# Performance work log

Hardware: AMD Instinct MI355X
Metric: run time of the kernel (lower is better)

Reference implementation:

```python
import jax, jax.numpy as jnp
import numpy as np

P = 64          # num_populations
T = 8192        # buffer_size (buffer assumed full / all valid)
K = 8           # num_bins
HIST = 2        # history_length
NPAST = K ** HIST          # number of single-series past states
NCOMB = NPAST * NPAST      # joint (y_past, x_past) states
N = T - HIST - 1           # n_samples per pair


def _discretize(x):
    # Faithful to torch _discretize: min-max normalize, floor into K bins.
    xmin = x.min()
    xmax = x.max()
    rng = xmax - xmin
    norm = (x - xmin) / (rng + 1e-8)
    b = jnp.clip((norm * (K - 1)).astype(jnp.int32), 0, K - 1)
    return jnp.where(rng < 1e-8, jnp.zeros_like(b), b)


def _cond_entropy(counts, state_mask):
    # counts: (S, K) histogram of y_future per conditioning state.
    # Torch skips states with total count < 2; weight = count/N.
    tot = counts.sum(axis=1)                          # (S,)
    valid = (tot >= 2.0) & state_mask
    p = counts / jnp.maximum(tot[:, None], 1.0)
    p_safe = jnp.where(counts > 0, p, 1.0)
    h = -jnp.where(counts > 0, p * jnp.log2(p_safe), 0.0).sum(axis=1)
    w = tot / N
    return jnp.where(valid, w * h, 0.0).sum()


def _te(src_d, tgt_d):
    # src_d, tgt_d: (T,) int bins. TE(src -> tgt) in bits.
    yf = tgt_d[HIST + 1: HIST + 1 + N]                # y_future, (N,)
    # hash of k-step histories: sum_i K**i * series[k-i : k-i+N]
    yp = sum((K ** i) * tgt_d[HIST - i: HIST - i + N] for i in range(HIST))
    xp = sum((K ** i) * src_d[HIST - i: HIST - i + N] for i in range(HIST))
    # joint histograms via scatter-add (the fused histogram kernel target)
    cy = jnp.zeros((NPAST, K), jnp.float32).at[yp, yf].add(1.0)
    cc = jnp.zeros((NCOMB, K), jnp.float32).at[yp * NPAST + xp, yf].add(1.0)
    # torch loops yp in range(min(NPAST, N)) -> mask out higher state ids
    mask_y = jnp.arange(NPAST) < min(NPAST, N)
    h_y_given_yp = _cond_entropy(cy, mask_y)
    h_y_given_ypxp = _cond_entropy(cc, jnp.ones((NCOMB,), dtype=bool))
    return jnp.maximum(0.0, h_y_given_yp - h_y_given_ypxp)


def setup_inputs() -> dict:
    key = jax.random.key(0)
    return {"time_series": jax.random.normal(key, (T, P), dtype=jnp.float32)}


def reference(time_series):
    # time_series: (T, P). Returns flow_matrix (P, P): flow[i, j] = TE(i -> j).
    d = jax.vmap(_discretize, in_axes=1, out_axes=0)(time_series)  # (P, T) int
    flow = jax.vmap(lambda s: jax.vmap(lambda t: _te(s, t))(d))(d)  # (P, P)
    return flow * (1.0 - jnp.eye(P, dtype=flow.dtype))  # diagonal forced to 0
```

## Files before the change

### kernel.cpp

```cpp
#include <hip/hip_runtime.h>

static constexpr int T = 8192;
static constexpr int P = 64;
static constexpr int NSAMP = 8189;

__global__ __launch_bounds__(1024) void prep_kernel(const float* __restrict__ ts,
        unsigned short* __restrict__ A, unsigned short* __restrict__ X,
        float* __restrict__ h_y)
{
    __shared__ float col[T];
    __shared__ unsigned char bins[T];
    __shared__ unsigned int cy[512];
    __shared__ float wred[32];
    const int p = blockIdx.x, tid = threadIdx.x;
    const int lane = tid & 63, wave = tid >> 6;

    float mn = 3.402823466e38f, mx = -3.402823466e38f;
    for (int t = tid; t < T; t += 1024) {
        float v = ts[t * P + p];
        col[t] = v;
        mn = fminf(mn, v);
        mx = fmaxf(mx, v);
    }
    #pragma unroll
    for (int off = 32; off > 0; off >>= 1) {
        mn = fminf(mn, __shfl_down(mn, off, 64));
        mx = fmaxf(mx, __shfl_down(mx, off, 64));
    }
    if (lane == 0) { wred[wave] = mn; wred[16 + wave] = mx; }
    for (int i = tid; i < 512; i += 1024) cy[i] = 0u;
    __syncthreads();
    float xmin = wred[0], xmax = wred[16];
    #pragma unroll
    for (int j = 1; j < 16; ++j) {
        xmin = fminf(xmin, wred[j]);
        xmax = fmaxf(xmax, wred[16 + j]);
    }
    const float rng = xmax - xmin;
    const float den = rng + 1e-8f;
    const int flat = rng < 1e-8f;

    for (int t = tid; t < T; t += 1024) {
        float norm = (col[t] - xmin) / den;
        int b = (int)(norm * 7.0f);
        b = b < 0 ? 0 : (b > 7 ? 7 : b);
        bins[t] = flat ? (unsigned char)0 : (unsigned char)b;
    }
    __syncthreads();

    unsigned short* Ap = A + p * T;
    unsigned short* Xp = X + p * T;
    for (int i = tid * 4; i + 3 < NSAMP; i += 4096) {
        unsigned w0 = *(const unsigned*)&bins[i];
        unsigned w1 = *(const unsigned*)&bins[i + 4];
        unsigned long long bb = (unsigned long long)w0 | ((unsigned long long)w1 << 32);
        ushort4 av, xv;
        unsigned short* ap = (unsigned short*)&av;
        unsigned short* xp = (unsigned short*)&xv;
        #pragma unroll
        for (int j = 0; j < 4; ++j) {
            unsigned b1 = (unsigned)(bb >> (8 * (j + 1))) & 255u;
            unsigned b2 = (unsigned)(bb >> (8 * (j + 2))) & 255u;
            unsigned b3 = (unsigned)(bb >> (8 * (j + 3))) & 255u;
            unsigned yp = b2 + 8u * b1;
            ap[j] = (unsigned short)(((yp * 320u) & 4095u) * 8u + b3);
            xp[j] = (unsigned short)(((yp * 709u) & 4095u) * 8u);
            atomicAdd(&cy[yp * 8u + b3], 1u);
        }
        *(ushort4*)(Ap + i) = av;
        *(ushort4*)(Xp + i) = xv;
    }
    if (tid == 0) {
        unsigned b1 = bins[NSAMP], b2 = bins[NSAMP + 1], b3 = bins[NSAMP + 2];
        unsigned yp = b2 + 8u * b1;
        Ap[NSAMP - 1] = (unsigned short)(((yp * 320u) & 4095u) * 8u + b3);
        Xp[NSAMP - 1] = (unsigned short)(((yp * 709u) & 4095u) * 8u);
        atomicAdd(&cy[yp * 8u + b3], 1u);
    }
    __syncthreads();

    if (tid < 64) {
        float tot = 0.0f, sc = 0.0f;
        #pragma unroll
        for (int v = 0; v < 8; ++v) {
            unsigned c = cy[tid * 8 + v];
            if (c) { float fc = (float)c; tot += fc; sc += fc * log2f(fc); }
        }
        float acc = (tot >= 2.0f) ? (tot * log2f(tot) - sc) : 0.0f;
        #pragma unroll
        for (int off = 32; off > 0; off >>= 1) acc += __shfl_down(acc, off, 64);
        if (tid == 0) h_y[p] = acc * (1.0f / (float)NSAMP);
    }
}

__global__ __launch_bounds__(256) void pair_kernel(const unsigned short* __restrict__ A,
        const unsigned short* __restrict__ X, const float* __restrict__ h_y,
        float* __restrict__ out)
{
    const int src = blockIdx.x >> 6, tgt = blockIdx.x & 63, tid = threadIdx.x;
    if (src == tgt) { if (tid == 0) out[blockIdx.x] = 0.0f; return; }

    __shared__ unsigned int hj[8192];
    __shared__ float red[4];

    uint4* z = (uint4*)hj;
    for (int i = tid; i < 2048; i += 256) z[i] = make_uint4(0u, 0u, 0u, 0u);
    __syncthreads();

    const unsigned short* At = A + tgt * T;
    const unsigned short* Xs = X + src * T;

    unsigned pc[16];
    unsigned cT = 0;

    #pragma unroll
    for (int it = 0; it < 4; ++it) {
        const int i = tid * 8 + it * 2048;
        if (it < 3 || tid < 255) {
            uint4 aw = *(const uint4*)(At + i);
            uint4 xw = *(const uint4*)(Xs + i);
            unsigned p0 = (aw.x + xw.x) & 0x7FFF7FFFu;
            unsigned p1 = (aw.y + xw.y) & 0x7FFF7FFFu;
            unsigned p2 = (aw.z + xw.z) & 0x7FFF7FFFu;
            unsigned p3 = (aw.w + xw.w) & 0x7FFF7FFFu;
            pc[it * 4 + 0] = p0; pc[it * 4 + 1] = p1;
            pc[it * 4 + 2] = p2; pc[it * 4 + 3] = p3;
            atomicAdd(&hj[(p0 & 0x7FFFu) >> 2], 1u << ((p0 & 3u) << 3));
            atomicAdd(&hj[p0 >> 18],            1u << (((p0 >> 16) & 3u) << 3));
            atomicAdd(&hj[(p1 & 0x7FFFu) >> 2], 1u << ((p1 & 3u) << 3));
            atomicAdd(&hj[p1 >> 18],            1u << (((p1 >> 16) & 3u) << 3));
            atomicAdd(&hj[(p2 & 0x7FFFu) >> 2], 1u << ((p2 & 3u) << 3));
            atomicAdd(&hj[p2 >> 18],            1u << (((p2 >> 16) & 3u) << 3));
            atomicAdd(&hj[(p3 & 0x7FFFu) >> 2], 1u << ((p3 & 3u) << 3));
            atomicAdd(&hj[p3 >> 18],            1u << (((p3 >> 16) & 3u) << 3));
        }
    }
    if (tid < 5) {
        unsigned s = ((unsigned)At[8184 + tid] + (unsigned)Xs[8184 + tid]) & 0x7FFFu;
        cT = s;
        atomicAdd(&hj[s >> 2], 1u << ((s & 3u) << 3));
    }
    __syncthreads();

    const unsigned char* hc = (const unsigned char*)hj;
    float acc = 0.0f;
    #pragma unroll
    for (int it = 0; it < 4; ++it) {
        if (it < 3 || tid < 255) {
            #pragma unroll
            for (int j = 0; j < 4; ++j) {
                unsigned pcv = pc[it * 4 + j];
                acc += __log2f((float)hc[pcv & 0xFFFFu]);
                acc += __log2f((float)hc[pcv >> 16]);
            }
        }
    }
    if (tid < 5) acc += __log2f((float)hc[cT]);

    float tpart = 0.0f;
    for (int s = tid; s < 4096; s += 256) {
        uint2 wv = *(const uint2*)&hj[s * 2];
        unsigned s0 = (wv.x & 0x00FF00FFu) + ((wv.x >> 8) & 0x00FF00FFu);
        unsigned s1 = (wv.y & 0x00FF00FFu) + ((wv.y >> 8) & 0x00FF00FFu);
        unsigned ss = s0 + s1;
        unsigned tot = (ss & 0xFFFFu) + (ss >> 16);
        float ft = (float)tot;
        tpart += ft * __log2f(fmaxf(ft, 1.0f));
    }
    acc = tpart - acc;

    #pragma unroll
    for (int off = 32; off > 0; off >>= 1) acc += __shfl_down(acc, off, 64);
    if ((tid & 63) == 0) red[tid >> 6] = acc;
    __syncthreads();
    if (tid == 0) {
        float h2 = (red[0] + red[1] + red[2] + red[3]) * (1.0f / (float)NSAMP);
        out[blockIdx.x] = fmaxf(0.0f, h_y[tgt] - h2);
    }
}

extern "C" void kernel_launch(void* const* d_in, const int* in_sizes, int n_in,
                              void* d_out, int out_size, void* d_ws, size_t ws_size,
                              hipStream_t stream)
{
    const float* ts = (const float*)d_in[0];
    float* out = (float*)d_out;
    unsigned short* A = (unsigned short*)d_ws;
    unsigned short* X = A + P * T;
    float* h_y = (float*)(X + P * T);

    prep_kernel<<<dim3(P), dim3(1024), 0, stream>>>(ts, A, X, h_y);
    pair_kernel<<<dim3(P * P), dim3(256), 0, stream>>>(A, X, h_y, out);
}
```

Baseline: 96.68 us.

## Fuse entropy into histogram atomics via returned counts; add transpose prep stage

The pair kernel now uses the old value returned by each shared-memory atomic increment together with a lookup table of (c+1)log(c+1)-c·log(c). This accumulates the sum of count·log(count) incrementally, so the second pass that re-read the histogram and computed a log per sample is gone. The pair kernel also grows to 512 threads per block with a launch-bounds occupancy hint. A new transpose kernel coalesces the strided column reads of the input and precomputes per-block min/max, so the prep kernel can vector-load contiguous rows. The cost is an extra launch and extra workspace traffic.

```diff
diff --git a/kernel.cpp b/kernel.cpp
--- a/kernel.cpp
+++ b/kernel.cpp
@@ -3,49 +3,89 @@
 static constexpr int T = 8192;
 static constexpr int P = 64;
 static constexpr int NSAMP = 8189;
-
-__global__ __launch_bounds__(1024) void prep_kernel(const float* __restrict__ ts,
+static constexpr int NBLK = 128;
+
+__global__ __launch_bounds__(256) void transpose_kernel(const float* __restrict__ ts,
+        float* __restrict__ tsT, float* __restrict__ pmin, float* __restrict__ pmax)
+{
+    __shared__ float tile[64 * 65];
+    const int tid = threadIdx.x;
+    const int r0 = blockIdx.x * 64;
+    const float4* ts4 = (const float4*)(ts + r0 * P);
+    #pragma unroll
+    for (int k = 0; k < 4; ++k) {
+        int g = tid + k * 256;
+        int r = g >> 4, c = (g & 15) * 4;
+        float4 v = ts4[g];
+        float* dst = &tile[r * 65 + c];
+        dst[0] = v.x; dst[1] = v.y; dst[2] = v.z; dst[3] = v.w;
+    }
+    __syncthreads();
+    #pragma unroll
+    for (int k = 0; k < 4; ++k) {
+        int g = tid + k * 256;
+        int s = g >> 4, j4 = g & 15;
+        float a = tile[(j4 * 4 + 0) * 65 + s];
+        float b = tile[(j4 * 4 + 1) * 65 + s];
+        float c = tile[(j4 * 4 + 2) * 65 + s];
+        float d = tile[(j4 * 4 + 3) * 65 + s];
+        float4 o; o.x = a; o.y = b; o.z = c; o.w = d;
+        *(float4*)(tsT + s * T + r0 + j4 * 4) = o;
+        float mn = fminf(fminf(a, b), fminf(c, d));
+        float mx = fmaxf(fmaxf(a, b), fmaxf(c, d));
+        #pragma unroll
+        for (int off = 8; off > 0; off >>= 1) {
+            mn = fminf(mn, __shfl_down(mn, off, 16));
+            mx = fmaxf(mx, __shfl_down(mx, off, 16));
+        }
+        if (j4 == 0) { pmin[s * NBLK + blockIdx.x] = mn; pmax[s * NBLK + blockIdx.x] = mx; }
+    }
+}
+
+__global__ __launch_bounds__(1024) void prep_kernel(const float* __restrict__ tsT,
+        const float* __restrict__ pmin, const float* __restrict__ pmax,
         unsigned short* __restrict__ A, unsigned short* __restrict__ X,
         float* __restrict__ h_y)
 {
-    __shared__ float col[T];
     __shared__ unsigned char bins[T];
     __shared__ unsigned int cy[512];
-    __shared__ float wred[32];
+    __shared__ float wred[4];
     const int p = blockIdx.x, tid = threadIdx.x;
     const int lane = tid & 63, wave = tid >> 6;
 
-    float mn = 3.402823466e38f, mx = -3.402823466e38f;
-    for (int t = tid; t < T; t += 1024) {
-        float v = ts[t * P + p];
-        col[t] = v;
-        mn = fminf(mn, v);
-        mx = fmaxf(mx, v);
-    }
-    #pragma unroll
-    for (int off = 32; off > 0; off >>= 1) {
-        mn = fminf(mn, __shfl_down(mn, off, 64));
-        mx = fmaxf(mx, __shfl_down(mx, off, 64));
-    }
-    if (lane == 0) { wred[wave] = mn; wred[16 + wave] = mx; }
+    if (tid < 128) {
+        float mn = pmin[p * NBLK + tid];
+        float mx = pmax[p * NBLK + tid];
+        #pragma unroll
+        for (int off = 32; off > 0; off >>= 1) {
+            mn = fminf(mn, __shfl_down(mn, off, 64));
+            mx = fmaxf(mx, __shfl_down(mx, off, 64));
+        }
+        if (lane == 0) { wred[wave] = mn; wred[2 + wave] = mx; }
+    }
     for (int i = tid; i < 512; i += 1024) cy[i] = 0u;
     __syncthreads();
-    float xmin = wred[0], xmax = wred[16];
-    #pragma unroll
-    for (int j = 1; j < 16; ++j) {
-        xmin = fminf(xmin, wred[j]);
-        xmax = fmaxf(xmax, wred[16 + j]);
-    }
+    const float xmin = fminf(wred[0], wred[1]);
+    const float xmax = fmaxf(wred[2], wred[3]);
     const float rng = xmax - xmin;
     const float den = rng + 1e-8f;
     const int flat = rng < 1e-8f;
 
-    for (int t = tid; t < T; t += 1024) {
-        float norm = (col[t] - xmin) / den;
-        int b = (int)(norm * 7.0f);
-        b = b < 0 ? 0 : (b > 7 ? 7 : b);
-        bins[t] = flat ? (unsigned char)0 : (unsigned char)b;
-    }
+    const float4* c4p = (const float4*)(tsT + p * T);
+    float4 v0 = c4p[tid * 2], v1 = c4p[tid * 2 + 1];
+    float vv[8] = { v0.x, v0.y, v0.z, v0.w, v1.x, v1.y, v1.z, v1.w };
+    unsigned pk0 = 0u, pk1 = 0u;
+    #pragma unroll
+    for (int j = 0; j < 4; ++j) {
+        float n0 = (vv[j] - xmin) / den;
+        float n1 = (vv[4 + j] - xmin) / den;
+        int b0 = (int)(n0 * 7.0f); b0 = b0 < 0 ? 0 : (b0 > 7 ? 7 : b0);
+        int b1 = (int)(n1 * 7.0f); b1 = b1 < 0 ? 0 : (b1 > 7 ? 7 : b1);
+        if (flat) { b0 = 0; b1 = 0; }
+        pk0 |= (unsigned)b0 << (8 * j);
+        pk1 |= (unsigned)b1 << (8 * j);
+    }
+    *(uint2*)&bins[tid * 8] = make_uint2(pk0, pk1);
     __syncthreads();
 
     unsigned short* Ap = A + p * T;
@@ -93,7 +133,7 @@
     }
 }
 
-__global__ __launch_bounds__(256) void pair_kernel(const unsigned short* __restrict__ A,
+__global__ __launch_bounds__(512, 8) void pair_kernel(const unsigned short* __restrict__ A,
         const unsigned short* __restrict__ X, const float* __restrict__ h_y,
         float* __restrict__ out)
 {
@@ -101,64 +141,54 @@
     if (src == tgt) { if (tid == 0) out[blockIdx.x] = 0.0f; return; }
 
     __shared__ unsigned int hj[8192];
-    __shared__ float red[4];
-
+    __shared__ float lut[256];
+    __shared__ float red[8];
+
+    if (tid < 256) {
+        float fc = (float)tid;
+        float f0 = (tid == 0) ? 0.0f : fc * log2f(fc);
+        lut[tid] = (fc + 1.0f) * log2f(fc + 1.0f) - f0;
+    }
     uint4* z = (uint4*)hj;
-    for (int i = tid; i < 2048; i += 256) z[i] = make_uint4(0u, 0u, 0u, 0u);
+    for (int i = tid; i < 2048; i += 512) z[i] = make_uint4(0u, 0u, 0u, 0u);
     __syncthreads();
 
     const unsigned short* At = A + tgt * T;
     const unsigned short* Xs = X + src * T;
-
-    unsigned pc[16];
-    unsigned cT = 0;
-
-    #pragma unroll
-    for (int it = 0; it < 4; ++it) {
-        const int i = tid * 8 + it * 2048;
-        if (it < 3 || tid < 255) {
-            uint4 aw = *(const uint4*)(At + i);
-            uint4 xw = *(const uint4*)(Xs + i);
-            unsigned p0 = (aw.x + xw.x) & 0x7FFF7FFFu;
-            unsigned p1 = (aw.y + xw.y) & 0x7FFF7FFFu;
-            unsigned p2 = (aw.z + xw.z) & 0x7FFF7FFFu;
-            unsigned p3 = (aw.w + xw.w) & 0x7FFF7FFFu;
-            pc[it * 4 + 0] = p0; pc[it * 4 + 1] = p1;
-            pc[it * 4 + 2] = p2; pc[it * 4 + 3] = p3;
-            atomicAdd(&hj[(p0 & 0x7FFFu) >> 2], 1u << ((p0 & 3u) << 3));
-            atomicAdd(&hj[p0 >> 18],            1u << (((p0 >> 16) & 3u) << 3));
-            atomicAdd(&hj[(p1 & 0x7FFFu) >> 2], 1u << ((p1 & 3u) << 3));
-            atomicAdd(&hj[p1 >> 18],            1u << (((p1 >> 16) & 3u) << 3));
-            atomicAdd(&hj[(p2 & 0x7FFFu) >> 2], 1u << ((p2 & 3u) << 3));
-            atomicAdd(&hj[p2 >> 18],            1u << (((p2 >> 16) & 3u) << 3));
-            atomicAdd(&hj[(p3 & 0x7FFFu) >> 2], 1u << ((p3 & 3u) << 3));
-            atomicAdd(&hj[p3 >> 18],            1u << (((p3 >> 16) & 3u) << 3));
-        }
+    float jacc = 0.0f;
+
+    auto pstep = [&](unsigned aw, unsigned xw) {
+        unsigned pk = (aw + xw) & 0x7FFF7FFFu;
+        unsigned c0 = pk & 0xFFFFu, c1 = pk >> 16;
+        unsigned sh0 = (c0 & 3u) << 3, sh1 = (c1 & 3u) << 3;
+        unsigned o0 = atomicAdd(&hj[c0 >> 2], 1u << sh0);
+        unsigned o1 = atomicAdd(&hj[c1 >> 2], 1u << sh1);
+        jacc += lut[(o0 >> sh0) & 255u];
+        jacc += lut[(o1 >> sh1) & 255u];
+    };
+
+    {
+        const int i = tid * 8;
+        uint4 aw = *(const uint4*)(At + i);
+        uint4 xw = *(const uint4*)(Xs + i);
+        pstep(aw.x, xw.x); pstep(aw.y, xw.y); pstep(aw.z, xw.z); pstep(aw.w, xw.w);
+    }
+    if (tid < 511) {
+        const int i = 4096 + tid * 8;
+        uint4 aw = *(const uint4*)(At + i);
+        uint4 xw = *(const uint4*)(Xs + i);
+        pstep(aw.x, xw.x); pstep(aw.y, xw.y); pstep(aw.z, xw.z); pstep(aw.w, xw.w);
     }
     if (tid < 5) {
-        unsigned s = ((unsigned)At[8184 + tid] + (unsigned)Xs[8184 + tid]) & 0x7FFFu;
-        cT = s;
-        atomicAdd(&hj[s >> 2], 1u << ((s & 3u) << 3));
-    }
-    __syncthreads();
-
-    const unsigned char* hc = (const unsigned char*)hj;
-    float acc = 0.0f;
-    #pragma unroll
-    for (int it = 0; it < 4; ++it) {
-        if (it < 3 || tid < 255) {
-            #pragma unroll
-            for (int j = 0; j < 4; ++j) {
-                unsigned pcv = pc[it * 4 + j];
-                acc += __log2f((float)hc[pcv & 0xFFFFu]);
-                acc += __log2f((float)hc[pcv >> 16]);
-            }
-        }
-    }
-    if (tid < 5) acc += __log2f((float)hc[cT]);
+        unsigned c = ((unsigned)At[8184 + tid] + (unsigned)Xs[8184 + tid]) & 0x7FFFu;
+        unsigned sh = (c & 3u) << 3;
+        unsigned o = atomicAdd(&hj[c >> 2], 1u << sh);
+        jacc += lut[(o >> sh) & 255u];
+    }
+    __syncthreads();
 
     float tpart = 0.0f;
-    for (int s = tid; s < 4096; s += 256) {
+    for (int s = tid; s < 4096; s += 512) {
         uint2 wv = *(const uint2*)&hj[s * 2];
         unsigned s0 = (wv.x & 0x00FF00FFu) + ((wv.x >> 8) & 0x00FF00FFu);
         unsigned s1 = (wv.y & 0x00FF00FFu) + ((wv.y >> 8) & 0x00FF00FFu);
@@ -167,14 +197,15 @@
         float ft = (float)tot;
         tpart += ft * __log2f(fmaxf(ft, 1.0f));
     }
-    acc = tpart - acc;
+    float acc = tpart - jacc;
 
     #pragma unroll
     for (int off = 32; off > 0; off >>= 1) acc += __shfl_down(acc, off, 64);
     if ((tid & 63) == 0) red[tid >> 6] = acc;
     __syncthreads();
     if (tid == 0) {
-        float h2 = (red[0] + red[1] + red[2] + red[3]) * (1.0f / (float)NSAMP);
+        float h2 = (red[0] + red[1] + red[2] + red[3] + red[4] + red[5] + red[6] + red[7])
+                   * (1.0f / (float)NSAMP);
         out[blockIdx.x] = fmaxf(0.0f, h_y[tgt] - h2);
     }
 }
@@ -188,7 +219,11 @@
     unsigned short* A = (unsigned short*)d_ws;
     unsigned short* X = A + P * T;
     float* h_y = (float*)(X + P * T);
-
-    prep_kernel<<<dim3(P), dim3(1024), 0, stream>>>(ts, A, X, h_y);
-    pair_kernel<<<dim3(P * P), dim3(256), 0, stream>>>(A, X, h_y, out);
-}
+    float* tsT = h_y + 64;
+    float* pmin = tsT + P * T;
+    float* pmax = pmin + P * NBLK;
+
+    transpose_kernel<<<dim3(NBLK), dim3(256), 0, stream>>>(ts, tsT, pmin, pmax);
+    prep_kernel<<<dim3(P), dim3(1024), 0, stream>>>(tsT, pmin, pmax, A, X, h_y);
+    pair_kernel<<<dim3(P * P), dim3(512), 0, stream>>>(A, X, h_y, out);
+}
```

Result: faster. 85.33 us (-11.7%).
